# Kernel optimization log

Hardware: AMD Instinct MI355X
Metric: run time of the kernel (lower is better)

## Reference

```python
import jax, jax.numpy as jnp
import numpy as np

ALPHA = 0.2  # leaky relu slope
NEG_BIG = -9000000000000000.0


def setup_inputs() -> dict:
    key = jax.random.key(0)
    k1, k2, k3, k4 = jax.random.split(key, 4)
    B, N, Fin, Fout = 8, 2048, 256, 256
    h = jax.random.normal(k1, (B, N, Fin), dtype=jnp.float32)
    adj = jax.random.randint(k2, (B, N, N), 0, 2, dtype=jnp.int32)
    # xavier_uniform with gain=1.414
    gain = 1.414
    limW = gain * np.sqrt(6.0 / (Fin + Fout))
    W = jax.random.uniform(k3, (Fin, Fout), dtype=jnp.float32, minval=-limW, maxval=limW)
    lima = gain * np.sqrt(6.0 / (2 * Fout + 1))
    a = jax.random.uniform(k4, (2 * Fout, 1), dtype=jnp.float32, minval=-lima, maxval=lima)
    return {"h": h, "adj": adj, "W": W, "a": a}


def reference(h, adj, W, a):
    # Wh: [B, N, F]
    Wh = jnp.matmul(h, W)
    Fout = W.shape[1]
    a1 = a[:Fout, 0]   # scores for source node i (repeat_interleave side)
    a2 = a[Fout:, 0]   # scores for target node j (repeat side)
    # e[b,i,j] = leakyrelu(Wh[b,i]@a1 + Wh[b,j]@a2)  -- decomposed, no O(N^2 * 2F) tensor
    s1 = jnp.einsum('bnf,f->bn', Wh, a1)  # [B, N]
    s2 = jnp.einsum('bnf,f->bn', Wh, a2)  # [B, N]
    e = jax.nn.leaky_relu(s1[:, :, None] + s2[:, None, :], negative_slope=ALPHA)
    masked = jnp.where(adj > 0, e, jnp.full_like(e, NEG_BIG))
    attention = jax.nn.softmax(masked, axis=2)  # dropout=0 (eval mode)
    h_prime = jnp.matmul(attention, Wh)  # [B, N, F]
    return jax.nn.elu(h_prime)
```

## Files before the change

kernel.cpp:

```cpp
#include <hip/hip_runtime.h>

typedef __attribute__((ext_vector_type(8))) short bhalf8;
typedef __attribute__((ext_vector_type(4))) float floatx4;

#define ALPHA_LR 0.2f

__device__ __forceinline__ unsigned short f2bf(float f) {
  union { float f; unsigned int u; } v; v.f = f;
  unsigned int r = v.u + 0x7fffu + ((v.u >> 16) & 1u);
  return (unsigned short)(r >> 16);
}
__device__ __forceinline__ float bf2f(unsigned short u) {
  union { unsigned int u; float f; } v; v.u = ((unsigned int)u) << 16;
  return v.f;
}
__device__ __forceinline__ void gld16(const void* g, void* l) {
  __builtin_amdgcn_global_load_lds((const __attribute__((address_space(1))) unsigned int*)g,
                                   (__attribute__((address_space(3))) unsigned int*)l,
                                   16, 0, 0);
}

__global__ void k0w_split(const float* __restrict__ W,
                          unsigned short* __restrict__ WThi,
                          unsigned short* __restrict__ WTlo,
                          unsigned int* __restrict__ s2maxEnc) {
  __shared__ float s[16][17];
  const int tx = threadIdx.x, ty = threadIdx.y;
  if (blockIdx.x == 0 && blockIdx.y == 0 && ty == 0 && tx < 8) s2maxEnc[tx] = 0u;
  const int n0 = blockIdx.x * 16, k0 = blockIdx.y * 16;
  s[ty][tx] = W[(k0 + ty) * 256 + n0 + tx];
  __syncthreads();
  float v = s[tx][ty];
  const int k = k0 + tx, n = n0 + ty;
  unsigned short hi = f2bf(v);
  unsigned short lo = f2bf(v - bf2f(hi));
  const int idx = (k >> 5) * 8192 + n * 32 + (k & 31);
  WThi[idx] = hi;
  WTlo[idx] = lo;
}

__global__ __launch_bounds__(512, 2) void k1_mfma(const float* __restrict__ h,
                                                  const unsigned short* __restrict__ Bhi_g,
                                                  const unsigned short* __restrict__ Blo_g,
                                                  const float* __restrict__ a_g,
                                                  unsigned short* __restrict__ WhPack,
                                                  float* __restrict__ s1,
                                                  float* __restrict__ s2,
                                                  unsigned int* __restrict__ s2maxEnc) {
  __shared__ unsigned short Ah[64 * 264], Al[64 * 264];
  __shared__ unsigned short Bh[2][8192], Bl[2][8192];
  __shared__ float s1red[64], s2red[64];
  const int t = threadIdx.x;
  const long r0 = (long)blockIdx.x * 64;
  const int wave = t >> 6, lane = t & 63;

  if (t < 64) { s1red[t] = 0.f; s2red[t] = 0.f; }

#pragma unroll
  for (int rep = 0; rep < 2; rep++) {
    const int off = wave * 1024 + rep * 512;
    gld16(Bhi_g + off + lane * 8, &Bh[0][off]);
    gld16(Blo_g + off + lane * 8, &Bl[0][off]);
  }

#pragma unroll
  for (int q = 0; q < 8; q++) {
    int idx = q * 512 + t;
    int row = idx >> 6, c4 = idx & 63;
    float4 x = *(const float4*)(h + (r0 + row) * 256 + c4 * 4);
    float xs[4] = {x.x, x.y, x.z, x.w};
    unsigned short hs[4], ls[4];
#pragma unroll
    for (int qq = 0; qq < 4; qq++) {
      hs[qq] = f2bf(xs[qq]);
      ls[qq] = f2bf(xs[qq] - bf2f(hs[qq]));
    }
    *(ushort4*)&Ah[row * 264 + c4 * 4] = (ushort4){hs[0], hs[1], hs[2], hs[3]};
    *(ushort4*)&Al[row * 264 + c4 * 4] = (ushort4){ls[0], ls[1], ls[2], ls[3]};
  }
  __syncthreads();

  const int wm = wave >> 2, wn = wave & 3;
  const int lhi = lane >> 4, llo = lane & 15;

  floatx4 acc[2][4];
#pragma unroll
  for (int mt = 0; mt < 2; mt++)
#pragma unroll
    for (int nt = 0; nt < 4; nt++) acc[mt][nt] = (floatx4){0.f, 0.f, 0.f, 0.f};

  for (int ks = 0; ks < 8; ks++) {
    const int cur = ks & 1, nxt = cur ^ 1, ksn = (ks + 1) & 7;
#pragma unroll
    for (int rep = 0; rep < 2; rep++) {
      const int off = wave * 1024 + rep * 512;
      gld16(Bhi_g + ksn * 8192 + off + lane * 8, &Bh[nxt][off]);
      gld16(Blo_g + ksn * 8192 + off + lane * 8, &Bl[nxt][off]);
    }

    const int k0 = ks * 32;
    bhalf8 ah[2], al[2], bh[4], bl[4];
#pragma unroll
    for (int mt = 0; mt < 2; mt++) {
      int ro = (wm * 32 + mt * 16 + llo) * 264 + k0 + lhi * 8;
      ah[mt] = *(const bhalf8*)&Ah[ro];
      al[mt] = *(const bhalf8*)&Al[ro];
    }
#pragma unroll
    for (int nt = 0; nt < 4; nt++) {
      int ro = (wn * 64 + nt * 16 + llo) * 32 + lhi * 8;
      bh[nt] = *(const bhalf8*)&Bh[cur][ro];
      bl[nt] = *(const bhalf8*)&Bl[cur][ro];
    }
#pragma unroll
    for (int mt = 0; mt < 2; mt++)
#pragma unroll
      for (int nt = 0; nt < 4; nt++) {
        acc[mt][nt] = __builtin_amdgcn_mfma_f32_16x16x32_bf16(ah[mt], bh[nt], acc[mt][nt], 0, 0, 0);
        acc[mt][nt] = __builtin_amdgcn_mfma_f32_16x16x32_bf16(ah[mt], bl[nt], acc[mt][nt], 0, 0, 0);
        acc[mt][nt] = __builtin_amdgcn_mfma_f32_16x16x32_bf16(al[mt], bh[nt], acc[mt][nt], 0, 0, 0);
      }
    __syncthreads();
  }

  float a1v[4], a2v[4];
#pragma unroll
  for (int nt = 0; nt < 4; nt++) {
    int f = wn * 64 + nt * 16 + llo;
    a1v[nt] = a_g[f];
    a2v[nt] = a_g[256 + f];
  }

  const int b = (int)(r0 >> 11);
  const int jt_base = (int)((r0 & 2047) >> 5);

#pragma unroll
  for (int mt = 0; mt < 2; mt++) {
    float p1[4], p2[4];
#pragma unroll
    for (int reg = 0; reg < 4; reg++) {
      p1[reg] = acc[mt][0][reg] * a1v[0] + acc[mt][1][reg] * a1v[1] +
                acc[mt][2][reg] * a1v[2] + acc[mt][3][reg] * a1v[3];
      p2[reg] = acc[mt][0][reg] * a2v[0] + acc[mt][1][reg] * a2v[1] +
                acc[mt][2][reg] * a2v[2] + acc[mt][3][reg] * a2v[3];
    }
#pragma unroll
    for (int off = 1; off < 16; off <<= 1) {
#pragma unroll
      for (int reg = 0; reg < 4; reg++) {
        p1[reg] += __shfl_xor(p1[reg], off);
        p2[reg] += __shfl_xor(p2[reg], off);
      }
    }
    if (llo == 0) {
#pragma unroll
      for (int reg = 0; reg < 4; reg++) {
        int il = wm * 32 + mt * 16 + lhi * 4 + reg;
        atomicAdd(&s1red[il], p1[reg]);
        atomicAdd(&s2red[il], p2[reg]);
      }
    }
#pragma unroll
    for (int nt = 0; nt < 4; nt++) {
      int f = wn * 64 + nt * 16 + llo;
      int jt = jt_base + wm;
      ushort4 pk = (ushort4){f2bf(acc[mt][nt][0]), f2bf(acc[mt][nt][1]),
                             f2bf(acc[mt][nt][2]), f2bf(acc[mt][nt][3])};
      *(ushort4*)&WhPack[((long)((b * 64 + jt) * 256 + f)) * 32 + mt * 16 + lhi * 4] = pk;
    }
  }

  __syncthreads();
  if (t < 64) {
    s1[r0 + t] = s1red[t];
    s2[r0 + t] = s2red[t];
    float v = s2red[t];
#pragma unroll
    for (int o = 32; o; o >>= 1) v = fmaxf(v, __shfl_xor(v, o));
    if (t == 0) {
      unsigned int u = __float_as_uint(v);
      unsigned int key = (u & 0x80000000u) ? ~u : (u | 0x80000000u);
      atomicMax(s2maxEnc + b, key);
    }
  }
}

__global__ __launch_bounds__(512, 4) void k3_attn(const unsigned short* __restrict__ WhPack,
                                                  const int* __restrict__ adj,
                                                  const float* __restrict__ s1g,
                                                  const float* __restrict__ s2g,
                                                  const unsigned int* __restrict__ s2maxEnc,
                                                  float* __restrict__ out) {
  const int t = threadIdx.x;
  const int lin = blockIdx.y * 64 + blockIdx.x;
  const int b = lin & 7;
  const int i0 = (lin >> 3) * 32;
  const long gr0 = (long)b * 2048 + i0;

  __shared__ float s2all[2048];
  __shared__ unsigned short P[2][1280];
  __shared__ float lvv[32];

  ((float4*)s2all)[t] = ((const float4*)(s2g + (long)b * 2048))[t];

  const int wave = t >> 6, lane = t & 63;
  const int wm = wave >> 2, wn = wave & 3;
  const int lhi = lane >> 4, llo = lane & 15;
  const int i_p = t >> 4;
  const int jl0 = (t & 15) * 2;

  const float s1i = s1g[gr0 + i_p];
  const unsigned int ek = s2maxEnc[b];
  const float s2max = (ek & 0x80000000u) ? __uint_as_float(ek & 0x7fffffffu)
                                         : __uint_as_float(~ek);
  const float xm = s1i + s2max;
  const float Mi = fmaxf(xm, ALPHA_LR * xm);

  const int* aptr = adj + (gr0 + i_p) * 2048 + jl0;
  const unsigned short* wb = WhPack + ((long)b * 64) * 8192 + (wn * 64 + llo) * 32 + lhi * 8;

  int2 aj0 = *(const int2*)aptr;
  int2 aj1 = *(const int2*)(aptr + 32);
  bhalf8 bf[4];
#pragma unroll
  for (int nt = 0; nt < 4; nt++) bf[nt] = *(const bhalf8*)(wb + nt * 512);

  __syncthreads();

  float lsum;
  {
    float x0 = s1i + s2all[jl0];
    float x1 = s1i + s2all[jl0 + 1];
    x0 = fmaxf(x0, ALPHA_LR * x0);
    x1 = fmaxf(x1, ALPHA_LR * x1);
    float e0 = (aj0.x > 0) ? __expf(x0 - Mi) : 0.f;
    float e1 = (aj0.y > 0) ? __expf(x1 - Mi) : 0.f;
    lsum = e0 + e1;
    *(unsigned int*)&P[0][i_p * 40 + jl0] =
        (unsigned)f2bf(e0) | ((unsigned)f2bf(e1) << 16);
  }
  __syncthreads();

  floatx4 acc[4];
#pragma unroll
  for (int nt = 0; nt < 4; nt++) acc[nt] = (floatx4){0.f, 0.f, 0.f, 0.f};

#pragma unroll 2
  for (int jt = 0; jt < 64; jt++) {
    const int cur = jt & 1, nxt = cur ^ 1;
    bhalf8 bfn[4];
    if (jt < 63) {
      const int jtn = jt + 1;
      const long tb = (long)jtn * 8192;
#pragma unroll
      for (int nt = 0; nt < 4; nt++) bfn[nt] = *(const bhalf8*)(wb + tb + nt * 512);
      const int2 ajc = aj1;
      const int jpf = (jt + 2 < 64) ? jt + 2 : 63;
      aj1 = *(const int2*)(aptr + jpf * 32);
      float x0 = s1i + s2all[jtn * 32 + jl0];
      float x1 = s1i + s2all[jtn * 32 + jl0 + 1];
      x0 = fmaxf(x0, ALPHA_LR * x0);
      x1 = fmaxf(x1, ALPHA_LR * x1);
      float e0 = (ajc.x > 0) ? __expf(x0 - Mi) : 0.f;
      float e1 = (ajc.y > 0) ? __expf(x1 - Mi) : 0.f;
      lsum += e0 + e1;
      *(unsigned int*)&P[nxt][i_p * 40 + jl0] =
          (unsigned)f2bf(e0) | ((unsigned)f2bf(e1) << 16);
    }
    bhalf8 af = *(const bhalf8*)&P[cur][(wm * 16 + llo) * 40 + lhi * 8];
#pragma unroll
    for (int nt = 0; nt < 4; nt++)
      acc[nt] = __builtin_amdgcn_mfma_f32_16x16x32_bf16(af, bf[nt], acc[nt], 0, 0, 0);
    __syncthreads();
#pragma unroll
    for (int nt = 0; nt < 4; nt++) bf[nt] = bfn[nt];
  }

  lsum += __shfl_xor(lsum, 1);
  lsum += __shfl_xor(lsum, 2);
  lsum += __shfl_xor(lsum, 4);
  lsum += __shfl_xor(lsum, 8);
  if ((t & 15) == 0) lvv[i_p] = 1.f / fmaxf(lsum, 1e-35f);
  __syncthreads();

#pragma unroll
  for (int nt = 0; nt < 4; nt++) {
#pragma unroll
    for (int reg = 0; reg < 4; reg++) {
      int il = wm * 16 + lhi * 4 + reg;
      int f = wn * 64 + nt * 16 + llo;
      float v = acc[nt][reg] * lvv[il];
      v = v > 0.f ? v : expm1f(v);
      out[(gr0 + il) * 256 + f] = v;
    }
  }
}

extern "C" void kernel_launch(void* const* d_in, const int* in_sizes, int n_in,
                              void* d_out, int out_size, void* d_ws, size_t ws_size,
                              hipStream_t stream) {
  const float* h = (const float*)d_in[0];
  const int* adj = (const int*)d_in[1];
  const float* W = (const float*)d_in[2];
  const float* a = (const float*)d_in[3];
  float* out = (float*)d_out;

  char* ws = (char*)d_ws;
  unsigned short* WhPack = (unsigned short*)ws;
  unsigned short* WThi = (unsigned short*)(ws + 8388608);
  unsigned short* WTlo = (unsigned short*)(ws + 8519680);
  float* s1 = (float*)(ws + 8650752);
  float* s2 = (float*)(ws + 8716288);
  unsigned int* s2maxEnc = (unsigned int*)(ws + 8781824);

  hipLaunchKernelGGL(k0w_split, dim3(16, 16), dim3(16, 16), 0, stream, W, WThi, WTlo, s2maxEnc);
  hipLaunchKernelGGL(k1_mfma, dim3(256), dim3(512), 0, stream, h, WThi, WTlo, a,
                     WhPack, s1, s2, s2maxEnc);
  hipLaunchKernelGGL(k3_attn, dim3(64, 8), dim3(512), 0, stream, WhPack, adj,
                     s1, s2, s2maxEnc, out);
}
```

Measured before the change: 275.9 us.

## Process 128-column chunks per barrier with 2x2 MFMA tiles per wave

Restructures the attention kernel's main loop so each barrier step covers 128 key columns instead of 32. That cuts the number of __syncthreads from 64 to 16. Each wave now owns a 32-feature slice across all 32 rows, computing a 2x2 grid of MFMA tiles so A fragments from LDS are reused across two B tiles. Adjacency and s2 are loaded as 8-wide vectors with deeper prefetch, and the P buffer is padded to a 136 stride. The trade is more registers per thread (eight B fragments, more prefetched adj), which may reduce occupancy under launch_bounds(512,4).

```diff
diff --git a/kernel.cpp b/kernel.cpp
--- a/kernel.cpp
+++ b/kernel.cpp
@@ -1,6 +1,7 @@
 #include <hip/hip_runtime.h>
 
 typedef __attribute__((ext_vector_type(8))) short bhalf8;
+typedef __attribute__((ext_vector_type(8))) unsigned short ushort8v;
 typedef __attribute__((ext_vector_type(4))) float floatx4;
 
 #define ALPHA_LR 0.2f
@@ -198,16 +199,15 @@
   const long gr0 = (long)b * 2048 + i0;
 
   __shared__ float s2all[2048];
-  __shared__ unsigned short P[2][1280];
+  __shared__ unsigned short P[2][32 * 136];
   __shared__ float lvv[32];
 
   ((float4*)s2all)[t] = ((const float4*)(s2g + (long)b * 2048))[t];
 
   const int wave = t >> 6, lane = t & 63;
-  const int wm = wave >> 2, wn = wave & 3;
   const int lhi = lane >> 4, llo = lane & 15;
   const int i_p = t >> 4;
-  const int jl0 = (t & 15) * 2;
+  const int jl = (t & 15) * 8;
 
   const float s1i = s1g[gr0 + i_p];
   const unsigned int ek = s2maxEnc[b];
@@ -216,65 +216,94 @@
   const float xm = s1i + s2max;
   const float Mi = fmaxf(xm, ALPHA_LR * xm);
 
-  const int* aptr = adj + (gr0 + i_p) * 2048 + jl0;
-  const unsigned short* wb = WhPack + ((long)b * 64) * 8192 + (wn * 64 + llo) * 32 + lhi * 8;
-
-  int2 aj0 = *(const int2*)aptr;
-  int2 aj1 = *(const int2*)(aptr + 32);
-  bhalf8 bf[4];
-#pragma unroll
-  for (int nt = 0; nt < 4; nt++) bf[nt] = *(const bhalf8*)(wb + nt * 512);
-
-  __syncthreads();
-
-  float lsum;
+  const int* aptr = adj + (gr0 + i_p) * 2048 + jl;
+  const unsigned short* wb =
+      WhPack + ((long)b) * 524288 + (long)(wave * 1024 + llo * 32 + lhi * 8);
+
+  int4 ajP0 = *(const int4*)(aptr);
+  int4 ajP1 = *(const int4*)(aptr + 4);
+  int4 ajO0 = *(const int4*)(aptr + 128);
+  int4 ajO1 = *(const int4*)(aptr + 132);
+  int4 ajE0 = *(const int4*)(aptr + 256);
+  int4 ajE1 = *(const int4*)(aptr + 260);
+
+  bhalf8 bF[4][2];
+#pragma unroll
+  for (int tl = 0; tl < 4; tl++) {
+    bF[tl][0] = *(const bhalf8*)(wb + (long)tl * 8192);
+    bF[tl][1] = *(const bhalf8*)(wb + (long)tl * 8192 + 512);
+  }
+
+  __syncthreads();
+
+  float lsum = 0.f;
   {
-    float x0 = s1i + s2all[jl0];
-    float x1 = s1i + s2all[jl0 + 1];
-    x0 = fmaxf(x0, ALPHA_LR * x0);
-    x1 = fmaxf(x1, ALPHA_LR * x1);
-    float e0 = (aj0.x > 0) ? __expf(x0 - Mi) : 0.f;
-    float e1 = (aj0.y > 0) ? __expf(x1 - Mi) : 0.f;
-    lsum = e0 + e1;
-    *(unsigned int*)&P[0][i_p * 40 + jl0] =
-        (unsigned)f2bf(e0) | ((unsigned)f2bf(e1) << 16);
-  }
-  __syncthreads();
-
-  floatx4 acc[4];
-#pragma unroll
-  for (int nt = 0; nt < 4; nt++) acc[nt] = (floatx4){0.f, 0.f, 0.f, 0.f};
-
-#pragma unroll 2
-  for (int jt = 0; jt < 64; jt++) {
-    const int cur = jt & 1, nxt = cur ^ 1;
-    bhalf8 bfn[4];
-    if (jt < 63) {
-      const int jtn = jt + 1;
-      const long tb = (long)jtn * 8192;
-#pragma unroll
-      for (int nt = 0; nt < 4; nt++) bfn[nt] = *(const bhalf8*)(wb + tb + nt * 512);
-      const int2 ajc = aj1;
-      const int jpf = (jt + 2 < 64) ? jt + 2 : 63;
-      aj1 = *(const int2*)(aptr + jpf * 32);
-      float x0 = s1i + s2all[jtn * 32 + jl0];
-      float x1 = s1i + s2all[jtn * 32 + jl0 + 1];
-      x0 = fmaxf(x0, ALPHA_LR * x0);
-      x1 = fmaxf(x1, ALPHA_LR * x1);
-      float e0 = (ajc.x > 0) ? __expf(x0 - Mi) : 0.f;
-      float e1 = (ajc.y > 0) ? __expf(x1 - Mi) : 0.f;
-      lsum += e0 + e1;
-      *(unsigned int*)&P[nxt][i_p * 40 + jl0] =
-          (unsigned)f2bf(e0) | ((unsigned)f2bf(e1) << 16);
-    }
-    bhalf8 af = *(const bhalf8*)&P[cur][(wm * 16 + llo) * 40 + lhi * 8];
-#pragma unroll
-    for (int nt = 0; nt < 4; nt++)
-      acc[nt] = __builtin_amdgcn_mfma_f32_16x16x32_bf16(af, bf[nt], acc[nt], 0, 0, 0);
-    __syncthreads();
-#pragma unroll
-    for (int nt = 0; nt < 4; nt++) bf[nt] = bfn[nt];
-  }
+    float4 sA = *(const float4*)&s2all[jl];
+    float4 sB = *(const float4*)&s2all[jl + 4];
+    float xs[8] = {sA.x, sA.y, sA.z, sA.w, sB.x, sB.y, sB.z, sB.w};
+    int am[8] = {ajP0.x, ajP0.y, ajP0.z, ajP0.w, ajP1.x, ajP1.y, ajP1.z, ajP1.w};
+    unsigned short pe[8];
+#pragma unroll
+    for (int q = 0; q < 8; q++) {
+      float x = s1i + xs[q];
+      x = fmaxf(x, ALPHA_LR * x);
+      float e = (am[q] > 0) ? __expf(x - Mi) : 0.f;
+      lsum += e;
+      pe[q] = f2bf(e);
+    }
+    *(ushort8v*)&P[0][i_p * 136 + jl] =
+        (ushort8v){pe[0], pe[1], pe[2], pe[3], pe[4], pe[5], pe[6], pe[7]};
+  }
+  asm volatile("s_waitcnt lgkmcnt(0)\n\ts_barrier" ::: "memory");
+
+  floatx4 acc[2][2];
+#pragma unroll
+  for (int mt = 0; mt < 2; mt++)
+#pragma unroll
+    for (int nt = 0; nt < 2; nt++) acc[mt][nt] = (floatx4){0.f, 0.f, 0.f, 0.f};
+
+#define CHUNK_BODY(cc, AJ0, AJ1)                                                   \
+  {                                                                                \
+    const int cur = (cc) & 1, nxt = cur ^ 1;                                       \
+    if ((cc) < 15) {                                                               \
+      float4 sA = *(const float4*)&s2all[((cc) + 1) * 128 + jl];                   \
+      float4 sB = *(const float4*)&s2all[((cc) + 1) * 128 + jl + 4];               \
+      float xs[8] = {sA.x, sA.y, sA.z, sA.w, sB.x, sB.y, sB.z, sB.w};              \
+      int am[8] = {AJ0.x, AJ0.y, AJ0.z, AJ0.w, AJ1.x, AJ1.y, AJ1.z, AJ1.w};        \
+      unsigned short pe[8];                                                        \
+      _Pragma("unroll") for (int q = 0; q < 8; q++) {                              \
+        float x = s1i + xs[q];                                                     \
+        x = fmaxf(x, ALPHA_LR * x);                                                \
+        float e = (am[q] > 0) ? __expf(x - Mi) : 0.f;                              \
+        lsum += e;                                                                 \
+        pe[q] = f2bf(e);                                                           \
+      }                                                                            \
+      *(ushort8v*)&P[nxt][i_p * 136 + jl] =                                        \
+          (ushort8v){pe[0], pe[1], pe[2], pe[3], pe[4], pe[5], pe[6], pe[7]};      \
+    }                                                                              \
+    if ((cc) < 13) {                                                               \
+      AJ0 = *(const int4*)(aptr + ((cc) + 3) * 128);                               \
+      AJ1 = *(const int4*)(aptr + ((cc) + 3) * 128 + 4);                           \
+    }                                                                              \
+    const long jt4 = (long)((((cc) < 15) ? (cc) + 1 : 15) * 4) * 8192;             \
+    _Pragma("unroll") for (int tl = 0; tl < 4; tl++) {                             \
+      bhalf8 af0 = *(const bhalf8*)&P[cur][llo * 136 + tl * 32 + lhi * 8];         \
+      bhalf8 af1 = *(const bhalf8*)&P[cur][(16 + llo) * 136 + tl * 32 + lhi * 8];  \
+      acc[0][0] = __builtin_amdgcn_mfma_f32_16x16x32_bf16(af0, bF[tl][0], acc[0][0], 0, 0, 0); \
+      acc[0][1] = __builtin_amdgcn_mfma_f32_16x16x32_bf16(af0, bF[tl][1], acc[0][1], 0, 0, 0); \
+      acc[1][0] = __builtin_amdgcn_mfma_f32_16x16x32_bf16(af1, bF[tl][0], acc[1][0], 0, 0, 0); \
+      acc[1][1] = __builtin_amdgcn_mfma_f32_16x16x32_bf16(af1, bF[tl][1], acc[1][1], 0, 0, 0); \
+      bF[tl][0] = *(const bhalf8*)(wb + jt4 + (long)tl * 8192);                    \
+      bF[tl][1] = *(const bhalf8*)(wb + jt4 + (long)tl * 8192 + 512);              \
+    }                                                                              \
+    asm volatile("s_waitcnt lgkmcnt(0)\n\ts_barrier" ::: "memory");                \
+  }
+
+  for (int c2 = 0; c2 < 8; c2++) {
+    CHUNK_BODY(c2 * 2, ajO0, ajO1);
+    CHUNK_BODY(c2 * 2 + 1, ajE0, ajE1);
+  }
+#undef CHUNK_BODY
 
   lsum += __shfl_xor(lsum, 1);
   lsum += __shfl_xor(lsum, 2);
@@ -284,14 +313,17 @@
   __syncthreads();
 
 #pragma unroll
-  for (int nt = 0; nt < 4; nt++) {
-#pragma unroll
-    for (int reg = 0; reg < 4; reg++) {
-      int il = wm * 16 + lhi * 4 + reg;
-      int f = wn * 64 + nt * 16 + llo;
-      float v = acc[nt][reg] * lvv[il];
-      v = v > 0.f ? v : expm1f(v);
-      out[(gr0 + il) * 256 + f] = v;
+  for (int mt = 0; mt < 2; mt++) {
+#pragma unroll
+    for (int nt = 0; nt < 2; nt++) {
+#pragma unroll
+      for (int reg = 0; reg < 4; reg++) {
+        int il = mt * 16 + lhi * 4 + reg;
+        int f = wave * 32 + nt * 16 + llo;
+        float v = acc[mt][nt][reg] * lvv[il];
+        v = v > 0.f ? v : expm1f(v);
+        out[(gr0 + il) * 256 + f] = v;
+      }
     }
   }
 }
```

Result: faster. 255.1 us (-7.6%).

## Compute attention probabilities in MFMA registers, drop LDS staging and barriers

Applied to the files above, without the earlier changes.

The attention kernel now has each wave compute exp-scores straight into MFMA A-operand layout. Scores are packed to bf16 with v_cvt_pk_bf16_f32, which removes the shared-memory P double buffer, the s2 staging and all per-iteration __syncthreads. Each block now covers 64 rows: each wave handles two 16-row m-tiles, so every loaded B fragment is reused twice, and the grid shrinks to 256 blocks. Row sums are reduced with wave shuffles. In exchange there are more registers per thread (launch bounds lowered to 2 blocks per SM), fewer blocks to spread across CUs, and every wave redundantly recomputes exps for its own rows.

```diff
diff --git a/kernel.cpp b/kernel.cpp
--- a/kernel.cpp
+++ b/kernel.cpp
@@ -185,113 +185,125 @@
   }
 }
 
-__global__ __launch_bounds__(512, 4) void k3_attn(const unsigned short* __restrict__ WhPack,
+__global__ __launch_bounds__(512, 2) void k3_attn(const unsigned short* __restrict__ WhPack,
                                                   const int* __restrict__ adj,
                                                   const float* __restrict__ s1g,
                                                   const float* __restrict__ s2g,
                                                   const unsigned int* __restrict__ s2maxEnc,
                                                   float* __restrict__ out) {
   const int t = threadIdx.x;
-  const int lin = blockIdx.y * 64 + blockIdx.x;
+  const int lin = blockIdx.x;
   const int b = lin & 7;
-  const int i0 = (lin >> 3) * 32;
+  const int ig = lin >> 3;
+  const int wave = t >> 6, lane = t & 63;
+  const int rg = wave >> 2, fg = wave & 3;
+  const int i0 = ig * 64 + rg * 32;
   const long gr0 = (long)b * 2048 + i0;
-
-  __shared__ float s2all[2048];
-  __shared__ unsigned short P[2][1280];
-  __shared__ float lvv[32];
-
-  ((float4*)s2all)[t] = ((const float4*)(s2g + (long)b * 2048))[t];
-
-  const int wave = t >> 6, lane = t & 63;
-  const int wm = wave >> 2, wn = wave & 3;
-  const int lhi = lane >> 4, llo = lane & 15;
-  const int i_p = t >> 4;
-  const int jl0 = (t & 15) * 2;
-
-  const float s1i = s1g[gr0 + i_p];
+  const int llo = lane & 15, lhi = lane >> 4;
+
   const unsigned int ek = s2maxEnc[b];
   const float s2max = (ek & 0x80000000u) ? __uint_as_float(ek & 0x7fffffffu)
                                          : __uint_as_float(~ek);
-  const float xm = s1i + s2max;
-  const float Mi = fmaxf(xm, ALPHA_LR * xm);
-
-  const int* aptr = adj + (gr0 + i_p) * 2048 + jl0;
-  const unsigned short* wb = WhPack + ((long)b * 64) * 8192 + (wn * 64 + llo) * 32 + lhi * 8;
-
-  int2 aj0 = *(const int2*)aptr;
-  int2 aj1 = *(const int2*)(aptr + 32);
-  bhalf8 bf[4];
-#pragma unroll
-  for (int nt = 0; nt < 4; nt++) bf[nt] = *(const bhalf8*)(wb + nt * 512);
-
-  __syncthreads();
-
-  float lsum;
-  {
-    float x0 = s1i + s2all[jl0];
-    float x1 = s1i + s2all[jl0 + 1];
-    x0 = fmaxf(x0, ALPHA_LR * x0);
-    x1 = fmaxf(x1, ALPHA_LR * x1);
-    float e0 = (aj0.x > 0) ? __expf(x0 - Mi) : 0.f;
-    float e1 = (aj0.y > 0) ? __expf(x1 - Mi) : 0.f;
-    lsum = e0 + e1;
-    *(unsigned int*)&P[0][i_p * 40 + jl0] =
-        (unsigned)f2bf(e0) | ((unsigned)f2bf(e1) << 16);
-  }
-  __syncthreads();
-
-  floatx4 acc[4];
-#pragma unroll
-  for (int nt = 0; nt < 4; nt++) acc[nt] = (floatx4){0.f, 0.f, 0.f, 0.f};
-
-#pragma unroll 2
+  float s1i[2], Mi[2];
+#pragma unroll
+  for (int mt = 0; mt < 2; mt++) {
+    s1i[mt] = s1g[gr0 + mt * 16 + llo];
+    float xm = s1i[mt] + s2max;
+    Mi[mt] = fmaxf(xm, ALPHA_LR * xm);
+  }
+
+  const float* s2p = s2g + (long)b * 2048 + lhi * 8;
+  const int* ap0 = adj + (gr0 + llo) * 2048 + lhi * 8;
+  const int* ap1 = ap0 + 16 * 2048;
+  const unsigned short* wb =
+      WhPack + (long)b * 524288 + (long)((fg * 64 + llo) * 32 + lhi * 8);
+
+  int4 ajA0 = *(const int4*)ap0, ajB0 = *(const int4*)(ap0 + 4);
+  int4 ajA1 = *(const int4*)ap1, ajB1 = *(const int4*)(ap1 + 4);
+  float4 s2A = *(const float4*)s2p;
+  float4 s2B = *(const float4*)(s2p + 4);
+  bhalf8 bF[4];
+#pragma unroll
+  for (int nt = 0; nt < 4; nt++) bF[nt] = *(const bhalf8*)(wb + nt * 512);
+
+  floatx4 acc[2][4];
+#pragma unroll
+  for (int mt = 0; mt < 2; mt++)
+#pragma unroll
+    for (int nt = 0; nt < 4; nt++) acc[mt][nt] = (floatx4){0.f, 0.f, 0.f, 0.f};
+  float ls0 = 0.f, ls1 = 0.f;
+
   for (int jt = 0; jt < 64; jt++) {
-    const int cur = jt & 1, nxt = cur ^ 1;
-    bhalf8 bfn[4];
-    if (jt < 63) {
-      const int jtn = jt + 1;
-      const long tb = (long)jtn * 8192;
-#pragma unroll
-      for (int nt = 0; nt < 4; nt++) bfn[nt] = *(const bhalf8*)(wb + tb + nt * 512);
-      const int2 ajc = aj1;
-      const int jpf = (jt + 2 < 64) ? jt + 2 : 63;
-      aj1 = *(const int2*)(aptr + jpf * 32);
-      float x0 = s1i + s2all[jtn * 32 + jl0];
-      float x1 = s1i + s2all[jtn * 32 + jl0 + 1];
-      x0 = fmaxf(x0, ALPHA_LR * x0);
-      x1 = fmaxf(x1, ALPHA_LR * x1);
-      float e0 = (ajc.x > 0) ? __expf(x0 - Mi) : 0.f;
-      float e1 = (ajc.y > 0) ? __expf(x1 - Mi) : 0.f;
-      lsum += e0 + e1;
-      *(unsigned int*)&P[nxt][i_p * 40 + jl0] =
-          (unsigned)f2bf(e0) | ((unsigned)f2bf(e1) << 16);
-    }
-    bhalf8 af = *(const bhalf8*)&P[cur][(wm * 16 + llo) * 40 + lhi * 8];
+    const int jn = (jt < 63) ? jt + 1 : 63;
+    int4 anA0 = *(const int4*)(ap0 + jn * 32);
+    int4 anB0 = *(const int4*)(ap0 + jn * 32 + 4);
+    int4 anA1 = *(const int4*)(ap1 + jn * 32);
+    int4 anB1 = *(const int4*)(ap1 + jn * 32 + 4);
+    float4 s2nA = *(const float4*)(s2p + jn * 32);
+    float4 s2nB = *(const float4*)(s2p + jn * 32 + 4);
+    bhalf8 bFn[4];
 #pragma unroll
     for (int nt = 0; nt < 4; nt++)
-      acc[nt] = __builtin_amdgcn_mfma_f32_16x16x32_bf16(af, bf[nt], acc[nt], 0, 0, 0);
-    __syncthreads();
-#pragma unroll
-    for (int nt = 0; nt < 4; nt++) bf[nt] = bfn[nt];
-  }
-
-  lsum += __shfl_xor(lsum, 1);
-  lsum += __shfl_xor(lsum, 2);
-  lsum += __shfl_xor(lsum, 4);
-  lsum += __shfl_xor(lsum, 8);
-  if ((t & 15) == 0) lvv[i_p] = 1.f / fmaxf(lsum, 1e-35f);
-  __syncthreads();
-
-#pragma unroll
-  for (int nt = 0; nt < 4; nt++) {
+      bFn[nt] = *(const bhalf8*)(wb + (long)jn * 8192 + nt * 512);
+
+    bhalf8 pa[2];
+#pragma unroll
+    for (int mt = 0; mt < 2; mt++) {
+      const float s1v = s1i[mt], miv = Mi[mt];
+      const int4 aA = mt ? ajA1 : ajA0;
+      const int4 aB = mt ? ajB1 : ajB0;
+      float xs[8] = {s2A.x, s2A.y, s2A.z, s2A.w, s2B.x, s2B.y, s2B.z, s2B.w};
+      int am[8] = {aA.x, aA.y, aA.z, aA.w, aB.x, aB.y, aB.z, aB.w};
+      float e[8];
+      float lsm = 0.f;
+#pragma unroll
+      for (int q = 0; q < 8; q++) {
+        float x = s1v + xs[q];
+        float lk = fmaxf(x, ALPHA_LR * x);
+        float ee = __expf(lk - miv);
+        ee = (am[q] > 0) ? ee : 0.f;
+        lsm += ee;
+        e[q] = ee;
+      }
+      if (mt) ls1 += lsm; else ls0 += lsm;
+      union { unsigned int u[4]; bhalf8 v; } pk;
+#pragma unroll
+      for (int q = 0; q < 4; q++)
+        asm("v_cvt_pk_bf16_f32 %0, %1, %2" : "=v"(pk.u[q]) : "v"(e[2 * q]), "v"(e[2 * q + 1]));
+      pa[mt] = pk.v;
+    }
+
+#pragma unroll
+    for (int mt = 0; mt < 2; mt++)
+#pragma unroll
+      for (int nt = 0; nt < 4; nt++)
+        acc[mt][nt] = __builtin_amdgcn_mfma_f32_16x16x32_bf16(mt ? pa[1] : pa[0],
+                                                              bF[nt], acc[mt][nt], 0, 0, 0);
+
+    ajA0 = anA0; ajB0 = anB0; ajA1 = anA1; ajB1 = anB1;
+    s2A = s2nA; s2B = s2nB;
+#pragma unroll
+    for (int nt = 0; nt < 4; nt++) bF[nt] = bFn[nt];
+  }
+
+  ls0 += __shfl_xor(ls0, 16); ls0 += __shfl_xor(ls0, 32);
+  ls1 += __shfl_xor(ls1, 16); ls1 += __shfl_xor(ls1, 32);
+  float inv0 = 1.f / fmaxf(ls0, 1e-35f);
+  float inv1 = 1.f / fmaxf(ls1, 1e-35f);
+
+#pragma unroll
+  for (int mt = 0; mt < 2; mt++) {
 #pragma unroll
     for (int reg = 0; reg < 4; reg++) {
-      int il = wm * 16 + lhi * 4 + reg;
-      int f = wn * 64 + nt * 16 + llo;
-      float v = acc[nt][reg] * lvv[il];
-      v = v > 0.f ? v : expm1f(v);
-      out[(gr0 + il) * 256 + f] = v;
+      const int rloc = lhi * 4 + reg;
+      float iv = __shfl(mt ? inv1 : inv0, rloc);
+      const long orow = (gr0 + mt * 16 + rloc) * 256 + fg * 64 + llo;
+#pragma unroll
+      for (int nt = 0; nt < 4; nt++) {
+        float v = acc[mt][nt][reg] * iv;
+        v = v > 0.f ? v : expm1f(v);
+        out[orow + nt * 16] = v;
+      }
     }
   }
 }
@@ -316,6 +328,6 @@
   hipLaunchKernelGGL(k0w_split, dim3(16, 16), dim3(16, 16), 0, stream, W, WThi, WTlo, s2maxEnc);
   hipLaunchKernelGGL(k1_mfma, dim3(256), dim3(512), 0, stream, h, WThi, WTlo, a,
                      WhPack, s1, s2, s2maxEnc);
-  hipLaunchKernelGGL(k3_attn, dim3(64, 8), dim3(512), 0, stream, WhPack, adj,
+  hipLaunchKernelGGL(k3_attn, dim3(256), dim3(512), 0, stream, WhPack, adj,
                      s1, s2, s2maxEnc, out);
 }
```

Result: no change. 278.0 us (+0.8%).
